# Kernel optimization log

Measured on AMD Instinct MI355X. Metric: run time of the kernel, lower is better.

Reference implementation:

```python
import jax, jax.numpy as jnp
import numpy as np

B, C, T = 128, 19, 1000

def _conv2d(x, w, pad, groups=1):
    return jax.lax.conv_general_dilated(x, w, (1, 1), [(pad[0], pad[0]), (pad[1], pad[1])],
                                        dimension_numbers=('NCHW', 'OIHW', 'NCHW'),
                                        feature_group_count=groups)

def _conv1d(x, w, pad):
    return jax.lax.conv_general_dilated(x, w, (1,), [(pad, pad)],
                                        dimension_numbers=('NCH', 'OIH', 'NCH'))

def _bn(x, g, b, axis=1):
    # eval-mode BatchNorm with running_mean=0, running_var=1 -> pure affine
    shp = [1] * x.ndim
    shp[axis] = -1
    return x * g.reshape(shp) + b.reshape(shp)

def _gat(x, W, a_src, a_dst, bias, src, dst, ew):
    # GATConv, concat=False (head mean); messages scaled by external edge weight ew
    N = x.shape[0]
    H, D = a_src.shape
    h = (x @ W).reshape(N, H, D)
    e = jax.nn.leaky_relu((h * a_src).sum(-1)[src] + (h * a_dst).sum(-1)[dst], 0.2)  # [E,H]
    emax = jax.ops.segment_max(e, dst, num_segments=N)
    ee = jnp.exp(e - emax[dst])
    alpha = ee / (jax.ops.segment_sum(ee, dst, num_segments=N)[dst] + 1e-16)
    msg = (alpha * ew[:, None])[:, :, None] * h[src]  # [E,H,D]
    return jax.ops.segment_sum(msg, dst, num_segments=N).mean(1) + bias

def setup_inputs():
    key = jax.random.key(0)
    ks = iter(jax.random.split(key, 48))
    def nrm(shape, s=0.1):
        return jax.random.normal(next(ks), shape, jnp.float32) * s
    ii = np.arange(C)
    base = np.arange(B)[:, None] * C
    src = (base + np.repeat(ii, C)[None, :]).reshape(-1)
    dst = (base + np.tile(ii, C)[None, :]).reshape(-1)
    return {
        'x': nrm((B, C, T), 1.0),
        'conv1_w': nrm((16, 1, 1, 25)),
        'bn1_g': 1.0 + nrm((16,)), 'bn1_b': nrm((16,)),
        'depth_w': nrm((16, 1, C, 1)),
        'bn2_g': 1.0 + nrm((16,)), 'bn2_b': nrm((16,)),
        'se_w1': nrm((16, 4)), 'se_w2': nrm((4, 16)),
        'sep_w': nrm((16, 16, 1, 16)),
        'bn3_g': 1.0 + nrm((16,)), 'bn3_b': nrm((16,)),
        'ms_w0': nrm((16, 1, 15)), 'ms_g0': 1.0 + nrm((16,)), 'ms_b0': nrm((16,)),
        'ms_w1': nrm((16, 1, 25)), 'ms_g1': 1.0 + nrm((16,)), 'ms_b1': nrm((16,)),
        'ms_w2': nrm((16, 1, 35)), 'ms_g2': 1.0 + nrm((16,)), 'ms_b2': nrm((16,)),
        'adj_w': nrm((32, 1)), 'adj_b': nrm((1,)),
        'gat1_w': nrm((32, 8 * 64), 0.05), 'gat1_as': nrm((8, 64)), 'gat1_ad': nrm((8, 64)), 'gat1_bias': nrm((64,)),
        'skip1_w': nrm((32, 64)), 'skip1_b': nrm((64,)),
        'bng1_g': 1.0 + nrm((64,)), 'bng1_b': nrm((64,)),
        'gat2_w': nrm((64, 8 * 64), 0.05), 'gat2_as': nrm((8, 64)), 'gat2_ad': nrm((8, 64)), 'gat2_bias': nrm((64,)),
        'bng2_g': 1.0 + nrm((64,)), 'bng2_b': nrm((64,)),
        'cls_w1': nrm((64, 64)), 'cls_b1': nrm((64,)),
        'cls_w2': nrm((64, 2)), 'cls_b2': nrm((2,)),
        'edge_index': jnp.asarray(np.stack([src, dst]), dtype=jnp.int32),
        'batch_idx': jnp.repeat(jnp.arange(B, dtype=jnp.int32), C),
    }

def reference(x, conv1_w, bn1_g, bn1_b, depth_w, bn2_g, bn2_b, se_w1, se_w2, sep_w, bn3_g, bn3_b,
              ms_w0, ms_g0, ms_b0, ms_w1, ms_g1, ms_b1, ms_w2, ms_g2, ms_b2,
              adj_w, adj_b, gat1_w, gat1_as, gat1_ad, gat1_bias, skip1_w, skip1_b, bng1_g, bng1_b,
              gat2_w, gat2_as, gat2_ad, gat2_bias, bng2_g, bng2_b, cls_w1, cls_b1, cls_w2, cls_b2,
              edge_index, batch_idx):
    Bn, Cn, Tn = x.shape
    gelu = lambda v: jax.nn.gelu(v, approximate=False)
    # --- EEGNet-style frontend ---
    y = _conv2d(x[:, None], conv1_w, (0, 12))                 # [B,16,C,T]
    y = _bn(y, bn1_g, bn1_b)
    y = _conv2d(y, depth_w, (0, 0), groups=16)                # depthwise over channels -> [B,16,1,T]
    y = jax.nn.elu(_bn(y, bn2_g, bn2_b))
    s = y.mean((2, 3))                                        # SE squeeze [B,16]
    s = jax.nn.sigmoid(gelu(s @ se_w1) @ se_w2)
    y = y * s[:, :, None, None]
    y = y.reshape(Bn, 16, 1, Tn // 4, 4).mean(-1)             # AvgPool2d((1,4))
    y = jax.nn.elu(_bn(_conv2d(y, sep_w, (0, 8)), bn3_g, bn3_b))
    yv = y.mean((2, 3))                                       # AdaptiveAvgPool2d((C,1)): 1->C replicates
    y_nodes = jnp.broadcast_to(yv[:, None, :], (Bn, Cn, 16)).reshape(Bn * Cn, 16)
    # --- per-channel multiscale conv1d ---
    z = x.reshape(Bn * Cn, 1, Tn)
    acc = jax.nn.elu(_bn(_conv1d(z, ms_w0, 7), ms_g0, ms_b0))
    acc = acc + jax.nn.elu(_bn(_conv1d(z, ms_w1, 12), ms_g1, ms_b1))
    acc = acc + jax.nn.elu(_bn(_conv1d(z, ms_w2, 17), ms_g2, ms_b2))
    z = (acc / 3.0).mean(-1)                                  # AdaptiveAvgPool1d(1) -> [N,16]
    feat = jnp.concatenate([y_nodes, z], axis=1)              # [N,32]
    # --- edge-weighted GAT stack ---
    scores = jax.nn.sigmoid(feat @ adj_w + adj_b).reshape(-1)
    src, dst = edge_index[0], edge_index[1]
    ew = scores[src] * scores[dst]
    h = _gat(feat, gat1_w, gat1_as, gat1_ad, gat1_bias, src, dst, ew)
    h = gelu(_bn(h, bng1_g, bng1_b) + feat @ skip1_w + skip1_b)
    h2 = _gat(h, gat2_w, gat2_as, gat2_ad, gat2_bias, src, dst, ew)
    h = gelu(_bn(h2, bng2_g, bng2_b) + h2)
    # --- global mean pool + classifier ---
    gs = jax.ops.segment_sum(h, batch_idx, num_segments=Bn)
    cnt = jax.ops.segment_sum(jnp.ones((Bn * Cn, 1), h.dtype), batch_idx, num_segments=Bn)
    g = gs / cnt
    return gelu(g @ cls_w1 + cls_b1) @ cls_w2 + cls_b2
```

## Files before the change

### kernel.cpp

```cpp
#include <hip/hip_runtime.h>
#include <hip/hip_bf16.h>
#include <math.h>

#define BATCH 128
#define NCH 19
#define TLEN 1000
#define NNODES (BATCH * NCH)

__device__ __forceinline__ float eluf(float x) { return x > 0.f ? x : __expf(x) - 1.f; }
__device__ __forceinline__ float geluf(float x) { return 0.5f * x * (1.f + erff(x * 0.70710678118654752f)); }
__device__ __forceinline__ float sigf(float x) { return 1.f / (1.f + __expf(-x)); }
__device__ __forceinline__ float lrelu(float x) { return x > 0.f ? x : 0.2f * x; }

__global__ __launch_bounds__(256) void k_pool(
    const float* __restrict__ x, const float* __restrict__ w1,
    const float* __restrict__ bn1g, const float* __restrict__ bn1b,
    const float* __restrict__ dw, const float* __restrict__ bn2g,
    const float* __restrict__ bn2b, float* __restrict__ y4g,
    float* __restrict__ ssum) {
  int blk = blockIdx.x;
  int b = blk >> 4, f = blk & 15;
  int tid = threadIdx.x;
  __shared__ float xw[1024];
  __shared__ float dws[19], w1s[25];
  __shared__ float redw[4];
  if (tid < 19) dws[tid] = dw[f * 19 + tid];
  else if (tid >= 32 && tid < 57) w1s[tid - 32] = w1[f * 25 + tid - 32];
  __syncthreads();
  const float* xb = x + (size_t)b * NCH * TLEN;
  for (int i = tid; i < 1024; i += 256) {
    int t = i - 12;
    float v = 0.f;
    if (t >= 0 && t < TLEN) {
#pragma unroll
      for (int c = 0; c < 19; c++) v += dws[c] * xb[c * TLEN + t];
    }
    xw[i] = v;
  }
  __syncthreads();
  float g1 = bn1g[f], b1 = bn1b[f];
  float g2 = bn2g[f], b2 = bn2b[f];
  float sumdw = 0.f;
#pragma unroll
  for (int c = 0; c < 19; c++) sumdw += dws[c];
  float scale = g2 * g1, cb = g2 * b1 * sumdw + b2;
  float part = 0.f;
  if (tid < 250) {
    float pool = 0.f;
#pragma unroll
    for (int q = 0; q < 4; q++) {
      int t = 4 * tid + q;
      float acc = 0.f;
#pragma unroll
      for (int k = 0; k < 25; k++) acc += w1s[k] * xw[t + k];
      pool += eluf(scale * acc + cb);
    }
    part = pool;
    y4g[(size_t)(b * 16 + f) * 250 + tid] = pool * 0.25f;
  }
  int lane = tid & 63, wid = tid >> 6;
  for (int off = 32; off > 0; off >>= 1) part += __shfl_down(part, off, 64);
  if (lane == 0) redw[wid] = part;
  __syncthreads();
  if (tid == 0) ssum[b * 16 + f] = redw[0] + redw[1] + redw[2] + redw[3];
}

__global__ __launch_bounds__(256) void k_sep(
    const float* __restrict__ y4g, const float* __restrict__ ssum,
    const float* __restrict__ sew1, const float* __restrict__ sew2,
    const float* __restrict__ sw, const float* __restrict__ g3,
    const float* __restrict__ b3, float* __restrict__ yv) {
  int blk = blockIdx.x;
  int b = blk >> 4, fo = blk & 15;
  int tid = threadIdx.x;
  __shared__ float yloc[16 * 268];
  __shared__ float sws[256];
  __shared__ float s_s[16], se_s[16], u4[4];
  __shared__ float redw[4];
  sws[tid] = sw[fo * 256 + tid];
  if (tid < 16) s_s[tid] = ssum[b * 16 + tid] * (1.f / 1000.f);
  __syncthreads();
  if (tid < 4) {
    float a = 0.f;
#pragma unroll
    for (int ff = 0; ff < 16; ff++) a += s_s[ff] * sew1[ff * 4 + tid];
    u4[tid] = geluf(a);
  }
  __syncthreads();
  if (tid < 16) {
    float a = 0.f;
#pragma unroll
    for (int j = 0; j < 4; j++) a += u4[j] * sew2[j * 16 + tid];
    se_s[tid] = sigf(a);
  }
  __syncthreads();
#pragma unroll
  for (int fi = 0; fi < 16; fi++) {
    float sc = se_s[fi];
    const float* yr = y4g + (size_t)(b * 16 + fi) * 250;
    for (int j = tid; j < 268; j += 256) {
      float v = (j >= 8 && j < 258) ? yr[j - 8] * sc : 0.f;
      yloc[fi * 268 + j] = v;
    }
  }
  __syncthreads();
  float accsum = 0.f;
  if (tid < 251) {
    float acc = 0.f;
#pragma unroll
    for (int fi = 0; fi < 16; fi++) {
      const float* yr = &yloc[fi * 268 + tid];
      const float* wp = &sws[fi * 16];
#pragma unroll
      for (int k = 0; k < 16; k++) acc += yr[k] * wp[k];
    }
    accsum = eluf(g3[fo] * acc + b3[fo]);
  }
  int lane = tid & 63, wid = tid >> 6;
  for (int off = 32; off > 0; off >>= 1)
    accsum += __shfl_down(accsum, off, 64);
  if (lane == 0) redw[wid] = accsum;
  __syncthreads();
  if (tid == 0)
    yv[b * 16 + fo] = (redw[0] + redw[1] + redw[2] + redw[3]) * (1.f / 251.f);
}

__global__ __launch_bounds__(256) void k_ms(
    const float* __restrict__ x, const float* __restrict__ w0,
    const float* __restrict__ ga0, const float* __restrict__ bb0,
    const float* __restrict__ w1, const float* __restrict__ ga1,
    const float* __restrict__ bb1, const float* __restrict__ w2,
    const float* __restrict__ ga2, const float* __restrict__ bb2,
    const float* __restrict__ yv, float* __restrict__ feat) {
  int n = blockIdx.x, tid = threadIdx.x;
  int lane = tid & 63, wid = tid >> 6;
  __shared__ __align__(16) float xr[1040];
  __shared__ float red_s[16];
  for (int i = tid; i < 1040; i += 256) {
    int t = i - 17;
    xr[i] = (t >= 0 && t < TLEN) ? x[(size_t)n * TLEN + t] : 0.f;
  }
  __syncthreads();

  for (int fg = 0; fg < 4; fg++) {
    int fu = __builtin_amdgcn_readfirstlane(wid * 4 + fg);
    float wa[15], wb[25], wc[35];
#pragma unroll
    for (int k = 0; k < 15; k++) wa[k] = w0[fu * 15 + k];
#pragma unroll
    for (int k = 0; k < 25; k++) wb[k] = w1[fu * 25 + k];
#pragma unroll
    for (int k = 0; k < 35; k++) wc[k] = w2[fu * 35 + k];
    float g0 = ga0[fu], c0 = bb0[fu];
    float g1 = ga1[fu], c1 = bb1[fu];
    float g2 = ga2[fu], c2 = bb2[fu];

    float z = 0.f;
    for (int tb = 0; tb < TLEN; tb += 256) {
      int t0 = tb + lane * 4;
      int rb = t0 <= 996 ? t0 : 996;
      float4 xq[10];
      const float4* xp = reinterpret_cast<const float4*>(&xr[rb]);
#pragma unroll
      for (int i = 0; i < 10; i++) xq[i] = xp[i];
      float xv[40];
#pragma unroll
      for (int i = 0; i < 10; i++) {
        xv[4 * i] = xq[i].x; xv[4 * i + 1] = xq[i].y;
        xv[4 * i + 2] = xq[i].z; xv[4 * i + 3] = xq[i].w;
      }
#pragma unroll
      for (int q = 0; q < 4; q++) {
        if (t0 + q < TLEN) {
          float a0 = 0.f, a1 = 0.f, a2 = 0.f;
#pragma unroll
          for (int k = 0; k < 15; k++) a0 += xv[q + 10 + k] * wa[k];
#pragma unroll
          for (int k = 0; k < 25; k++) a1 += xv[q + 5 + k] * wb[k];
#pragma unroll
          for (int k = 0; k < 35; k++) a2 += xv[q + k] * wc[k];
          z += eluf(g0 * a0 + c0) + eluf(g1 * a1 + c1) + eluf(g2 * a2 + c2);
        }
      }
    }
    for (int off = 32; off > 0; off >>= 1) z += __shfl_down(z, off, 64);
    if (lane == 0) red_s[fu] = z;
  }
  __syncthreads();
  if (tid < 16) {
    feat[(size_t)n * 32 + 16 + tid] = red_s[tid] * (1.f / 3000.f);
    feat[(size_t)n * 32 + tid] = yv[(n / 19) * 16 + tid];
  }
}

__global__ __launch_bounds__(256) void k_gat(
    const float* __restrict__ feat, const float* __restrict__ adjw,
    const float* __restrict__ adjb, const float* __restrict__ g1w,
    const float* __restrict__ g1as, const float* __restrict__ g1ad,
    const float* __restrict__ g1bias, const float* __restrict__ skw,
    const float* __restrict__ skb, const float* __restrict__ bg1,
    const float* __restrict__ bb1, const float* __restrict__ g2w,
    const float* __restrict__ g2as, const float* __restrict__ g2ad,
    const float* __restrict__ g2bias, const float* __restrict__ bg2,
    const float* __restrict__ bb2, const float* __restrict__ cw1,
    const float* __restrict__ cb1, const float* __restrict__ cw2,
    const float* __restrict__ cb2, float* __restrict__ out) {
  int b = blockIdx.x, tid = threadIdx.x;
  __shared__ float fb[19 * 32];
  __shared__ float h1[19 * 512];
  __shared__ float as_s[19 * 8], ad_s[19 * 8], sc_s[19];
  __shared__ float watt[19 * 8 * 19];
  __shared__ float hb[19 * 64];
  __shared__ float hout[19 * 64];
  __shared__ float gpool[64], u_s[64];

  for (int i = tid; i < 19 * 32; i += 256) fb[i] = feat[(size_t)b * 19 * 32 + i];
  __syncthreads();

  {
    float wc0[32], wc1[32];
#pragma unroll
    for (int c = 0; c < 32; c++) {
      wc0[c] = g1w[c * 512 + tid];
      wc1[c] = g1w[c * 512 + tid + 256];
    }
    for (int i = 0; i < 19; i++) {
      float frow[32];
#pragma unroll
      for (int c = 0; c < 32; c++) frow[c] = fb[i * 32 + c];
      float a0 = 0.f, a1 = 0.f;
#pragma unroll
      for (int c = 0; c < 32; c++) {
        a0 += frow[c] * wc0[c];
        a1 += frow[c] * wc1[c];
      }
      h1[i * 512 + tid] = a0;
      h1[i * 512 + tid + 256] = a1;
    }
  }
  if (tid < 19) {
    float a = adjb[0];
#pragma unroll
    for (int c = 0; c < 32; c++) a += fb[tid * 32 + c] * adjw[c];
    sc_s[tid] = sigf(a);
  }
  __syncthreads();

  if (tid < 152) {
    int i = tid / 8, h = tid & 7;
    float a = 0.f, d2 = 0.f;
#pragma unroll
    for (int d = 0; d < 64; d++) {
      float hv = h1[i * 512 + h * 64 + d];
      a += hv * g1as[h * 64 + d];
      d2 += hv * g1ad[h * 64 + d];
    }
    as_s[tid] = a;
    ad_s[tid] = d2;
  }
  __syncthreads();
  if (tid < 152) {
    int j = tid / 8, h = tid & 7;
    float adj_ = ad_s[j * 8 + h];
    float ev[19], m = -1e30f;
#pragma unroll
    for (int i = 0; i < 19; i++) {
      float e = lrelu(as_s[i * 8 + h] + adj_);
      ev[i] = e;
      m = fmaxf(m, e);
    }
    float den = 0.f;
#pragma unroll
    for (int i = 0; i < 19; i++) {
      ev[i] = __expf(ev[i] - m);
      den += ev[i];
    }
    float inv = 1.f / (den + 1e-16f);
    float scj = sc_s[j];
#pragma unroll
    for (int i = 0; i < 19; i++)
      watt[(j * 8 + h) * 19 + i] = ev[i] * inv * sc_s[i] * scj;
  }
  __syncthreads();
  for (int idx = tid; idx < 19 * 64; idx += 256) {
    int j = idx >> 6, d = idx & 63;
    float acc = 0.f;
#pragma unroll
    for (int h = 0; h < 8; h++) {
      const float* wr = &watt[(j * 8 + h) * 19];
      float a = 0.f;
#pragma unroll
      for (int i = 0; i < 19; i++) a += wr[i] * h1[i * 512 + h * 64 + d];
      acc += a;
    }
    float om = acc * 0.125f + g1bias[d];
    float v = bg1[d] * om + bb1[d];
    float sk = skb[d];
    const float* fr = &fb[j * 32];
#pragma unroll
    for (int c = 0; c < 32; c++) sk += fr[c] * skw[c * 64 + d];
    hb[idx] = geluf(v + sk);
  }
  __syncthreads();

#pragma unroll
  for (int oo = 0; oo < 2; oo++) {
    int o = tid + oo * 256;
    float wc[64];
#pragma unroll
    for (int c = 0; c < 64; c++) wc[c] = g2w[c * 512 + o];
    for (int i = 0; i < 19; i++) {
      float a = 0.f;
#pragma unroll
      for (int c = 0; c < 64; c++) a += hb[i * 64 + c] * wc[c];
      h1[i * 512 + o] = a;
    }
  }
  __syncthreads();

  if (tid < 152) {
    int i = tid / 8, h = tid & 7;
    float a = 0.f, d2 = 0.f;
#pragma unroll
    for (int d = 0; d < 64; d++) {
      float hv = h1[i * 512 + h * 64 + d];
      a += hv * g2as[h * 64 + d];
      d2 += hv * g2ad[h * 64 + d];
    }
    as_s[tid] = a;
    ad_s[tid] = d2;
  }
  __syncthreads();
  if (tid < 152) {
    int j = tid / 8, h = tid & 7;
    float adj_ = ad_s[j * 8 + h];
    float ev[19], m = -1e30f;
#pragma unroll
    for (int i = 0; i < 19; i++) {
      float e = lrelu(as_s[i * 8 + h] + adj_);
      ev[i] = e;
      m = fmaxf(m, e);
    }
    float den = 0.f;
#pragma unroll
    for (int i = 0; i < 19; i++) {
      ev[i] = __expf(ev[i] - m);
      den += ev[i];
    }
    float inv = 1.f / (den + 1e-16f);
    float scj = sc_s[j];
#pragma unroll
    for (int i = 0; i < 19; i++)
      watt[(j * 8 + h) * 19 + i] = ev[i] * inv * sc_s[i] * scj;
  }
  __syncthreads();
  for (int idx = tid; idx < 19 * 64; idx += 256) {
    int j = idx >> 6, d = idx & 63;
    float acc = 0.f;
#pragma unroll
    for (int h = 0; h < 8; h++) {
      const float* wr = &watt[(j * 8 + h) * 19];
      float a = 0.f;
#pragma unroll
      for (int i = 0; i < 19; i++) a += wr[i] * h1[i * 512 + h * 64 + d];
      acc += a;
    }
    float om = acc * 0.125f + g2bias[d];
    float v = bg2[d] * om + bb2[d] + om;
    hout[idx] = geluf(v);
  }
  __syncthreads();

  if (tid < 64) {
    float a = 0.f;
#pragma unroll
    for (int j = 0; j < 19; j++) a += hout[j * 64 + tid];
    gpool[tid] = a * (1.f / 19.f);
  }
  __syncthreads();
  if (tid < 64) {
    float a = cb1[tid];
#pragma unroll
    for (int d = 0; d < 64; d++) a += gpool[d] * cw1[d * 64 + tid];
    u_s[tid] = geluf(a);
  }
  __syncthreads();
  if (tid < 2) {
    float a = cb2[tid];
#pragma unroll
    for (int e = 0; e < 64; e++) a += u_s[e] * cw2[e * 2 + tid];
    out[b * 2 + tid] = a;
  }
}

extern "C" void kernel_launch(void* const* d_in, const int* in_sizes, int n_in,
                              void* d_out, int out_size, void* d_ws,
                              size_t ws_size, hipStream_t stream) {
  (void)in_sizes; (void)n_in; (void)out_size; (void)ws_size;
  const float* x = (const float*)d_in[0];
  const float* conv1_w = (const float*)d_in[1];
  const float* bn1_g = (const float*)d_in[2];
  const float* bn1_b = (const float*)d_in[3];
  const float* depth_w = (const float*)d_in[4];
  const float* bn2_g = (const float*)d_in[5];
  const float* bn2_b = (const float*)d_in[6];
  const float* se_w1 = (const float*)d_in[7];
  const float* se_w2 = (const float*)d_in[8];
  const float* sep_w = (const float*)d_in[9];
  const float* bn3_g = (const float*)d_in[10];
  const float* bn3_b = (const float*)d_in[11];
  const float* ms_w0 = (const float*)d_in[12];
  const float* ms_g0 = (const float*)d_in[13];
  const float* ms_b0 = (const float*)d_in[14];
  const float* ms_w1 = (const float*)d_in[15];
  const float* ms_g1 = (const float*)d_in[16];
  const float* ms_b1 = (const float*)d_in[17];
  const float* ms_w2 = (const float*)d_in[18];
  const float* ms_g2 = (const float*)d_in[19];
  const float* ms_b2 = (const float*)d_in[20];
  const float* adj_w = (const float*)d_in[21];
  const float* adj_b = (const float*)d_in[22];
  const float* gat1_w = (const float*)d_in[23];
  const float* gat1_as = (const float*)d_in[24];
  const float* gat1_ad = (const float*)d_in[25];
  const float* gat1_bias = (const float*)d_in[26];
  const float* skip1_w = (const float*)d_in[27];
  const float* skip1_b = (const float*)d_in[28];
  const float* bng1_g = (const float*)d_in[29];
  const float* bng1_b = (const float*)d_in[30];
  const float* gat2_w = (const float*)d_in[31];
  const float* gat2_as = (const float*)d_in[32];
  const float* gat2_ad = (const float*)d_in[33];
  const float* gat2_bias = (const float*)d_in[34];
  const float* bng2_g = (const float*)d_in[35];
  const float* bng2_b = (const float*)d_in[36];
  const float* cls_w1 = (const float*)d_in[37];
  const float* cls_b1 = (const float*)d_in[38];
  const float* cls_w2 = (const float*)d_in[39];
  const float* cls_b2 = (const float*)d_in[40];

  float* ws = (float*)d_ws;
  float* yv = ws;
  float* feat = ws + 2048;
  float* y4g = ws + 79872;
  float* ssum = ws + 591872;

  hipLaunchKernelGGL(k_pool, dim3(BATCH * 16), dim3(256), 0, stream,
                     x, conv1_w, bn1_g, bn1_b, depth_w, bn2_g, bn2_b, y4g, ssum);
  hipLaunchKernelGGL(k_sep, dim3(BATCH * 16), dim3(256), 0, stream,
                     y4g, ssum, se_w1, se_w2, sep_w, bn3_g, bn3_b, yv);
  hipLaunchKernelGGL(k_ms, dim3(NNODES), dim3(256), 0, stream,
                     x, ms_w0, ms_g0, ms_b0, ms_w1, ms_g1, ms_b1, ms_w2,
                     ms_g2, ms_b2, yv, feat);
  hipLaunchKernelGGL(k_gat, dim3(BATCH), dim3(256), 0, stream,
                     feat, adj_w, adj_b, gat1_w, gat1_as, gat1_ad, gat1_bias,
                     skip1_w, skip1_b, bng1_g, bng1_b, gat2_w, gat2_as,
                     gat2_ad, gat2_bias, bng2_g, bng2_b, cls_w1, cls_b1,
                     cls_w2, cls_b2, (float*)d_out);
}
```

Measured before the change: 407.3 us.

## Retile pool kernel over time chunks, move SE sum into sep, pad ms smem

The pool kernel now assigns each block one time chunk covering all 16 filters instead of one filter over the full sequence. This removes the 16-fold redundant reads of x and the depthwise recompute. The SE channel sums are no longer produced by the pool kernel; the sep kernel recomputes them from the loaded y4 tile and applies the SE scale per input filter during accumulation. The multiscale kernel pads its shared-memory row to avoid bank conflicts, computes 8 outputs per lane, forces weights into scalar registers with readfirstlane, and keeps its loops rolled to hold register pressure down. Risks include higher register pressure in k_ms and a grid for k_pool that is smaller than before.

```diff
diff --git a/kernel.cpp b/kernel.cpp
--- a/kernel.cpp
+++ b/kernel.cpp
@@ -11,65 +11,73 @@
 __device__ __forceinline__ float geluf(float x) { return 0.5f * x * (1.f + erff(x * 0.70710678118654752f)); }
 __device__ __forceinline__ float sigf(float x) { return 1.f / (1.f + __expf(-x)); }
 __device__ __forceinline__ float lrelu(float x) { return x > 0.f ? x : 0.2f * x; }
-
+__device__ __forceinline__ float rfl(float v) {
+  return __uint_as_float(__builtin_amdgcn_readfirstlane(__float_as_uint(v)));
+}
+
+#define PCH 5
+#define PT 200
+#define PTILE 224
 __global__ __launch_bounds__(256) void k_pool(
     const float* __restrict__ x, const float* __restrict__ w1,
     const float* __restrict__ bn1g, const float* __restrict__ bn1b,
     const float* __restrict__ dw, const float* __restrict__ bn2g,
-    const float* __restrict__ bn2b, float* __restrict__ y4g,
-    float* __restrict__ ssum) {
+    const float* __restrict__ bn2b, float* __restrict__ y4g) {
   int blk = blockIdx.x;
-  int b = blk >> 4, f = blk & 15;
+  int b = blk / PCH, ch = blk % PCH;
   int tid = threadIdx.x;
-  __shared__ float xw[1024];
-  __shared__ float dws[19], w1s[25];
-  __shared__ float redw[4];
-  if (tid < 19) dws[tid] = dw[f * 19 + tid];
-  else if (tid >= 32 && tid < 57) w1s[tid - 32] = w1[f * 25 + tid - 32];
-  __syncthreads();
-  const float* xb = x + (size_t)b * NCH * TLEN;
-  for (int i = tid; i < 1024; i += 256) {
-    int t = i - 12;
-    float v = 0.f;
-    if (t >= 0 && t < TLEN) {
-#pragma unroll
-      for (int c = 0; c < 19; c++) v += dws[c] * xb[c * TLEN + t];
-    }
-    xw[i] = v;
-  }
-  __syncthreads();
-  float g1 = bn1g[f], b1 = bn1b[f];
-  float g2 = bn2g[f], b2 = bn2b[f];
-  float sumdw = 0.f;
-#pragma unroll
-  for (int c = 0; c < 19; c++) sumdw += dws[c];
-  float scale = g2 * g1, cb = g2 * b1 * sumdw + b2;
-  float part = 0.f;
-  if (tid < 250) {
+  __shared__ float xs[19 * PTILE];
+  __shared__ float xwt[16 * PTILE];
+  __shared__ float dws[16 * 19], w1s[16 * 25];
+  __shared__ float sc_s[16], cb_s[16];
+  int tbase = PT * ch - 12;
+  for (int i = tid; i < 19 * PTILE; i += 256) {
+    int c = i / PTILE, j = i - c * PTILE;
+    int t = tbase + j;
+    xs[i] = (t >= 0 && t < TLEN) ? x[(size_t)b * NCH * TLEN + c * TLEN + t] : 0.f;
+  }
+  for (int i = tid; i < 304; i += 256) dws[i] = dw[i];
+  for (int i = tid; i < 400; i += 256) w1s[i] = w1[i];
+  __syncthreads();
+  if (tid < 16) {
+    float sumdw = 0.f;
+#pragma unroll
+    for (int c = 0; c < 19; c++) sumdw += dws[tid * 19 + c];
+    float g1 = bn1g[tid], b1 = bn1b[tid];
+    float g2 = bn2g[tid], b2 = bn2b[tid];
+    sc_s[tid] = g2 * g1;
+    cb_s[tid] = g2 * b1 * sumdw + b2;
+  }
+  for (int i = tid; i < 16 * PTILE; i += 256) {
+    int f = i / PTILE, j = i - f * PTILE;
+    float a = 0.f;
+#pragma unroll
+    for (int c = 0; c < 19; c++) a += dws[f * 19 + c] * xs[c * PTILE + j];
+    xwt[i] = a;
+  }
+  __syncthreads();
+  for (int o = tid; o < 800; o += 256) {
+    int f = o / 50, p = o - f * 50;
+    float scale = sc_s[f], cb = cb_s[f];
+    const float* wr = &w1s[f * 25];
+    const float* xw = &xwt[f * PTILE + 4 * p];
     float pool = 0.f;
 #pragma unroll
     for (int q = 0; q < 4; q++) {
-      int t = 4 * tid + q;
       float acc = 0.f;
 #pragma unroll
-      for (int k = 0; k < 25; k++) acc += w1s[k] * xw[t + k];
+      for (int k = 0; k < 25; k++) acc += wr[k] * xw[q + k];
       pool += eluf(scale * acc + cb);
     }
-    part = pool;
-    y4g[(size_t)(b * 16 + f) * 250 + tid] = pool * 0.25f;
-  }
-  int lane = tid & 63, wid = tid >> 6;
-  for (int off = 32; off > 0; off >>= 1) part += __shfl_down(part, off, 64);
-  if (lane == 0) redw[wid] = part;
-  __syncthreads();
-  if (tid == 0) ssum[b * 16 + f] = redw[0] + redw[1] + redw[2] + redw[3];
+    y4g[(size_t)(b * 16 + f) * 250 + 50 * ch + p] = pool * 0.25f;
+  }
 }
 
 __global__ __launch_bounds__(256) void k_sep(
-    const float* __restrict__ y4g, const float* __restrict__ ssum,
-    const float* __restrict__ sew1, const float* __restrict__ sew2,
-    const float* __restrict__ sw, const float* __restrict__ g3,
-    const float* __restrict__ b3, float* __restrict__ yv) {
+    const float* __restrict__ y4g, const float* __restrict__ sew1,
+    const float* __restrict__ sew2, const float* __restrict__ sw,
+    const float* __restrict__ g3, const float* __restrict__ b3,
+    float* __restrict__ yv) {
   int blk = blockIdx.x;
   int b = blk >> 4, fo = blk & 15;
   int tid = threadIdx.x;
@@ -78,7 +86,22 @@
   __shared__ float s_s[16], se_s[16], u4[4];
   __shared__ float redw[4];
   sws[tid] = sw[fo * 256 + tid];
-  if (tid < 16) s_s[tid] = ssum[b * 16 + tid] * (1.f / 1000.f);
+#pragma unroll
+  for (int fi = 0; fi < 16; fi++) {
+    const float* yr = y4g + (size_t)(b * 16 + fi) * 250;
+    for (int j = tid; j < 268; j += 256) {
+      yloc[fi * 268 + j] = (j >= 8 && j < 258) ? yr[j - 8] : 0.f;
+    }
+  }
+  __syncthreads();
+  {
+    int fi = tid >> 4, part = tid & 15;
+    float a = 0.f;
+    for (int p = part; p < 250; p += 16) a += yloc[fi * 268 + 8 + p];
+#pragma unroll
+    for (int off = 8; off > 0; off >>= 1) a += __shfl_down(a, off, 16);
+    if (part == 0) s_s[fi] = a * 0.004f;
+  }
   __syncthreads();
   if (tid < 4) {
     float a = 0.f;
@@ -92,16 +115,6 @@
 #pragma unroll
     for (int j = 0; j < 4; j++) a += u4[j] * sew2[j * 16 + tid];
     se_s[tid] = sigf(a);
-  }
-  __syncthreads();
-#pragma unroll
-  for (int fi = 0; fi < 16; fi++) {
-    float sc = se_s[fi];
-    const float* yr = y4g + (size_t)(b * 16 + fi) * 250;
-    for (int j = tid; j < 268; j += 256) {
-      float v = (j >= 8 && j < 258) ? yr[j - 8] * sc : 0.f;
-      yloc[fi * 268 + j] = v;
-    }
   }
   __syncthreads();
   float accsum = 0.f;
@@ -111,8 +124,10 @@
     for (int fi = 0; fi < 16; fi++) {
       const float* yr = &yloc[fi * 268 + tid];
       const float* wp = &sws[fi * 16];
-#pragma unroll
-      for (int k = 0; k < 16; k++) acc += yr[k] * wp[k];
+      float afi = 0.f;
+#pragma unroll
+      for (int k = 0; k < 16; k++) afi += yr[k] * wp[k];
+      acc += se_s[fi] * afi;
     }
     accsum = eluf(g3[fo] * acc + b3[fo]);
   }
@@ -125,6 +140,7 @@
     yv[b * 16 + fo] = (redw[0] + redw[1] + redw[2] + redw[3]) * (1.f / 251.f);
 }
 
+#define PHYS(i) ((i) + ((((i) >> 5)) << 2))
 __global__ __launch_bounds__(256) void k_ms(
     const float* __restrict__ x, const float* __restrict__ w0,
     const float* __restrict__ ga0, const float* __restrict__ bb0,
@@ -134,44 +150,42 @@
     const float* __restrict__ yv, float* __restrict__ feat) {
   int n = blockIdx.x, tid = threadIdx.x;
   int lane = tid & 63, wid = tid >> 6;
-  __shared__ __align__(16) float xr[1040];
+  __shared__ __align__(16) float xr[1172];
   __shared__ float red_s[16];
   for (int i = tid; i < 1040; i += 256) {
     int t = i - 17;
-    xr[i] = (t >= 0 && t < TLEN) ? x[(size_t)n * TLEN + t] : 0.f;
-  }
-  __syncthreads();
-
+    xr[PHYS(i)] = (t >= 0 && t < TLEN) ? x[(size_t)n * TLEN + t] : 0.f;
+  }
+  __syncthreads();
+
+#pragma unroll 1
   for (int fg = 0; fg < 4; fg++) {
     int fu = __builtin_amdgcn_readfirstlane(wid * 4 + fg);
     float wa[15], wb[25], wc[35];
 #pragma unroll
-    for (int k = 0; k < 15; k++) wa[k] = w0[fu * 15 + k];
-#pragma unroll
-    for (int k = 0; k < 25; k++) wb[k] = w1[fu * 25 + k];
-#pragma unroll
-    for (int k = 0; k < 35; k++) wc[k] = w2[fu * 35 + k];
-    float g0 = ga0[fu], c0 = bb0[fu];
-    float g1 = ga1[fu], c1 = bb1[fu];
-    float g2 = ga2[fu], c2 = bb2[fu];
+    for (int k = 0; k < 15; k++) wa[k] = rfl(w0[fu * 15 + k]);
+#pragma unroll
+    for (int k = 0; k < 25; k++) wb[k] = rfl(w1[fu * 25 + k]);
+#pragma unroll
+    for (int k = 0; k < 35; k++) wc[k] = rfl(w2[fu * 35 + k]);
+    float g0 = rfl(ga0[fu]), c0 = rfl(bb0[fu]);
+    float g1 = rfl(ga1[fu]), c1 = rfl(bb1[fu]);
+    float g2 = rfl(ga2[fu]), c2 = rfl(bb2[fu]);
 
     float z = 0.f;
-    for (int tb = 0; tb < TLEN; tb += 256) {
-      int t0 = tb + lane * 4;
-      int rb = t0 <= 996 ? t0 : 996;
-      float4 xq[10];
-      const float4* xp = reinterpret_cast<const float4*>(&xr[rb]);
-#pragma unroll
-      for (int i = 0; i < 10; i++) xq[i] = xp[i];
-      float xv[40];
-#pragma unroll
-      for (int i = 0; i < 10; i++) {
-        xv[4 * i] = xq[i].x; xv[4 * i + 1] = xq[i].y;
-        xv[4 * i + 2] = xq[i].z; xv[4 * i + 3] = xq[i].w;
-      }
-#pragma unroll
-      for (int q = 0; q < 4; q++) {
-        if (t0 + q < TLEN) {
+#pragma unroll 1
+    for (int tb = 0; tb < 1024; tb += 512) {
+      int t0 = tb + 8 * lane;
+      if (t0 <= 992) {
+        float xv[44];
+#pragma unroll
+        for (int j = 0; j < 11; j++) {
+          float4 q4 = *reinterpret_cast<const float4*>(&xr[PHYS(t0 + 4 * j)]);
+          xv[4 * j] = q4.x; xv[4 * j + 1] = q4.y;
+          xv[4 * j + 2] = q4.z; xv[4 * j + 3] = q4.w;
+        }
+#pragma unroll
+        for (int q = 0; q < 8; q++) {
           float a0 = 0.f, a1 = 0.f, a2 = 0.f;
 #pragma unroll
           for (int k = 0; k < 15; k++) a0 += xv[q + 10 + k] * wa[k];
@@ -443,12 +457,11 @@
   float* yv = ws;
   float* feat = ws + 2048;
   float* y4g = ws + 79872;
-  float* ssum = ws + 591872;
-
-  hipLaunchKernelGGL(k_pool, dim3(BATCH * 16), dim3(256), 0, stream,
-                     x, conv1_w, bn1_g, bn1_b, depth_w, bn2_g, bn2_b, y4g, ssum);
+
+  hipLaunchKernelGGL(k_pool, dim3(BATCH * PCH), dim3(256), 0, stream,
+                     x, conv1_w, bn1_g, bn1_b, depth_w, bn2_g, bn2_b, y4g);
   hipLaunchKernelGGL(k_sep, dim3(BATCH * 16), dim3(256), 0, stream,
-                     y4g, ssum, se_w1, se_w2, sep_w, bn3_g, bn3_b, yv);
+                     y4g, se_w1, se_w2, sep_w, bn3_g, bn3_b, yv);
   hipLaunchKernelGGL(k_ms, dim3(NNODES), dim3(256), 0, stream,
                      x, ms_w0, ms_g0, ms_b0, ms_w1, ms_g1, ms_b1, ms_w2,
                      ms_g2, ms_b2, yv, feat);
```

Result: faster. 374.0 us (-8.2%).

## Restructure multiscale conv to 8 outputs per lane with padded LDS layout

Applied to the files above, without the earlier changes.

The multiscale conv1d kernel now has each lane compute 8 consecutive outputs in two time halves, which removes the 4-iteration time loop and the per-output bounds checks. Shared memory gets a padded layout (4 extra floats every 32) to cut bank conflicts on the float4 window loads. Filter weights are made wave-uniform via readfirstlane so they can live in scalar registers. In exchange, register pressure rises sharply (two 44-float windows per lane), which risks spilling or lower occupancy.

```diff
diff --git a/kernel.cpp b/kernel.cpp
--- a/kernel.cpp
+++ b/kernel.cpp
@@ -11,6 +11,9 @@
 __device__ __forceinline__ float geluf(float x) { return 0.5f * x * (1.f + erff(x * 0.70710678118654752f)); }
 __device__ __forceinline__ float sigf(float x) { return 1.f / (1.f + __expf(-x)); }
 __device__ __forceinline__ float lrelu(float x) { return x > 0.f ? x : 0.2f * x; }
+__device__ __forceinline__ float rfl(float v) {
+  return __uint_as_float(__builtin_amdgcn_readfirstlane(__float_as_uint(v)));
+}
 
 __global__ __launch_bounds__(256) void k_pool(
     const float* __restrict__ x, const float* __restrict__ w1,
@@ -125,6 +128,7 @@
     yv[b * 16 + fo] = (redw[0] + redw[1] + redw[2] + redw[3]) * (1.f / 251.f);
 }
 
+#define PHYS(i) ((i) + ((((i) >> 5)) << 2))
 __global__ __launch_bounds__(256) void k_ms(
     const float* __restrict__ x, const float* __restrict__ w0,
     const float* __restrict__ ga0, const float* __restrict__ bb0,
@@ -134,55 +138,69 @@
     const float* __restrict__ yv, float* __restrict__ feat) {
   int n = blockIdx.x, tid = threadIdx.x;
   int lane = tid & 63, wid = tid >> 6;
-  __shared__ __align__(16) float xr[1040];
+  __shared__ __align__(16) float xr[1172];
   __shared__ float red_s[16];
   for (int i = tid; i < 1040; i += 256) {
     int t = i - 17;
-    xr[i] = (t >= 0 && t < TLEN) ? x[(size_t)n * TLEN + t] : 0.f;
-  }
-  __syncthreads();
-
+    xr[PHYS(i)] = (t >= 0 && t < TLEN) ? x[(size_t)n * TLEN + t] : 0.f;
+  }
+  __syncthreads();
+
+  int t0 = 8 * lane;
+  int tB = t0 + 512;
+  bool validB = (tB <= 992);
+  int rbB = validB ? tB : 992;
+
+#pragma unroll 1
   for (int fg = 0; fg < 4; fg++) {
     int fu = __builtin_amdgcn_readfirstlane(wid * 4 + fg);
     float wa[15], wb[25], wc[35];
 #pragma unroll
-    for (int k = 0; k < 15; k++) wa[k] = w0[fu * 15 + k];
-#pragma unroll
-    for (int k = 0; k < 25; k++) wb[k] = w1[fu * 25 + k];
-#pragma unroll
-    for (int k = 0; k < 35; k++) wc[k] = w2[fu * 35 + k];
-    float g0 = ga0[fu], c0 = bb0[fu];
-    float g1 = ga1[fu], c1 = bb1[fu];
-    float g2 = ga2[fu], c2 = bb2[fu];
-
-    float z = 0.f;
-    for (int tb = 0; tb < TLEN; tb += 256) {
-      int t0 = tb + lane * 4;
-      int rb = t0 <= 996 ? t0 : 996;
-      float4 xq[10];
-      const float4* xp = reinterpret_cast<const float4*>(&xr[rb]);
-#pragma unroll
-      for (int i = 0; i < 10; i++) xq[i] = xp[i];
-      float xv[40];
-#pragma unroll
-      for (int i = 0; i < 10; i++) {
-        xv[4 * i] = xq[i].x; xv[4 * i + 1] = xq[i].y;
-        xv[4 * i + 2] = xq[i].z; xv[4 * i + 3] = xq[i].w;
+    for (int k = 0; k < 15; k++) wa[k] = rfl(w0[fu * 15 + k]);
+#pragma unroll
+    for (int k = 0; k < 25; k++) wb[k] = rfl(w1[fu * 25 + k]);
+#pragma unroll
+    for (int k = 0; k < 35; k++) wc[k] = rfl(w2[fu * 35 + k]);
+    float g0 = rfl(ga0[fu]), c0 = rfl(bb0[fu]);
+    float g1 = rfl(ga1[fu]), c1 = rfl(bb1[fu]);
+    float g2 = rfl(ga2[fu]), c2 = rfl(bb2[fu]);
+
+    float xvA[44], xvB[44];
+#pragma unroll
+    for (int j = 0; j < 11; j++) {
+      float4 qa = *reinterpret_cast<const float4*>(&xr[PHYS(t0 + 4 * j)]);
+      float4 qb = *reinterpret_cast<const float4*>(&xr[PHYS(rbB + 4 * j)]);
+      xvA[4 * j] = qa.x; xvA[4 * j + 1] = qa.y;
+      xvA[4 * j + 2] = qa.z; xvA[4 * j + 3] = qa.w;
+      xvB[4 * j] = qb.x; xvB[4 * j + 1] = qb.y;
+      xvB[4 * j + 2] = qb.z; xvB[4 * j + 3] = qb.w;
+    }
+
+    float z = 0.f, zB = 0.f;
+#pragma unroll
+    for (int q = 0; q < 8; q++) {
+      float a0 = 0.f, a1 = 0.f, a2 = 0.f;
+      float b0 = 0.f, b1 = 0.f, b2 = 0.f;
+#pragma unroll
+      for (int k = 0; k < 15; k++) {
+        a0 += xvA[q + 10 + k] * wa[k];
+        b0 += xvB[q + 10 + k] * wa[k];
       }
 #pragma unroll
-      for (int q = 0; q < 4; q++) {
-        if (t0 + q < TLEN) {
-          float a0 = 0.f, a1 = 0.f, a2 = 0.f;
-#pragma unroll
-          for (int k = 0; k < 15; k++) a0 += xv[q + 10 + k] * wa[k];
-#pragma unroll
-          for (int k = 0; k < 25; k++) a1 += xv[q + 5 + k] * wb[k];
-#pragma unroll
-          for (int k = 0; k < 35; k++) a2 += xv[q + k] * wc[k];
-          z += eluf(g0 * a0 + c0) + eluf(g1 * a1 + c1) + eluf(g2 * a2 + c2);
-        }
+      for (int k = 0; k < 25; k++) {
+        a1 += xvA[q + 5 + k] * wb[k];
+        b1 += xvB[q + 5 + k] * wb[k];
       }
-    }
+#pragma unroll
+      for (int k = 0; k < 35; k++) {
+        a2 += xvA[q + k] * wc[k];
+        b2 += xvB[q + k] * wc[k];
+      }
+      z += eluf(g0 * a0 + c0) + eluf(g1 * a1 + c1) + eluf(g2 * a2 + c2);
+      zB += eluf(g0 * b0 + c0) + eluf(g1 * b1 + c1) + eluf(g2 * b2 + c2);
+    }
+    z += validB ? zB : 0.f;
+
     for (int off = 32; off > 0; off >>= 1) z += __shfl_down(z, off, 64);
     if (lane == 0) red_s[fu] = z;
   }
```

New measurement: 449.2 us. 10.3% more time.
